# Performance work log

Hardware: AMD Instinct MI355X
Metric: run time of the kernel (lower is better)

## Reference

```python
import jax, jax.numpy as jnp
import numpy as np

N, E, B = 25600, 307200, 256
H, D, F0, K = 256, 16, 7, 6
GNN_OUT, TDA_IN, TDA_OUT, MEG_IN, MEG_OUT = 192, 32, 128, 16, 64
FUSION = GNN_OUT + TDA_OUT + MEG_OUT  # 384
MID = FUSION // 2  # 192


def _ln(x, g, b, eps=1e-5):
    m = x.mean(-1, keepdims=True)
    v = x.var(-1, keepdims=True)
    return (x - m) * jax.lax.rsqrt(v + eps) * g + b


def _ntn(x, pos, neg):
    return jnp.nan_to_num(x, nan=0.0, posinf=pos, neginf=neg)


def setup_inputs():
    key = jax.random.key(0)
    ks = iter(jax.random.split(key, 80))
    p = lambda *s: 0.05 * jax.random.normal(next(ks), s, jnp.float32)
    inp = {
        "x": jax.random.normal(next(ks), (N, F0), jnp.float32),
        "edge_attr": jax.random.uniform(next(ks), (E, D), dtype=jnp.float32),
        "tda": jax.random.normal(next(ks), (B, TDA_IN), jnp.float32),
        "megnet": jax.random.normal(next(ks), (B, MEG_IN), jnp.float32),
        "edge_index": jax.random.randint(next(ks), (2, E), 0, N),
        "batch": jnp.repeat(jnp.arange(B), N // B),
        # GNN encoder
        "gin_W": p(F0, H), "gin_b": jnp.zeros(H),
        "conv_Wf": p(6, 2 * H + D, H), "conv_bf": jnp.zeros((6, H)),
        "conv_Ws": p(6, 2 * H + D, H), "conv_bs": jnp.zeros((6, H)),
        "gln_g": jnp.ones((6, H)), "gln_b": jnp.zeros((6, H)),
        "gout_W": p(H, GNN_OUT), "gout_b": jnp.zeros(GNN_OUT),
        # TDA projector 32->256->256->128
        "t1_W": p(TDA_IN, 2 * TDA_OUT), "t1_b": jnp.zeros(2 * TDA_OUT),
        "tln1_g": jnp.ones(2 * TDA_OUT), "tln1_b": jnp.zeros(2 * TDA_OUT),
        "t2_W": p(2 * TDA_OUT, 2 * TDA_OUT), "t2_b": jnp.zeros(2 * TDA_OUT),
        "tln2_g": jnp.ones(2 * TDA_OUT), "tln2_b": jnp.zeros(2 * TDA_OUT),
        "t3_W": p(2 * TDA_OUT, TDA_OUT), "t3_b": jnp.zeros(TDA_OUT),
        # MEGNet projector 16->128->128->64
        "m1_W": p(MEG_IN, 2 * MEG_OUT), "m1_b": jnp.zeros(2 * MEG_OUT),
        "mln1_g": jnp.ones(2 * MEG_OUT), "mln1_b": jnp.zeros(2 * MEG_OUT),
        "m2_W": p(2 * MEG_OUT, 2 * MEG_OUT), "m2_b": jnp.zeros(2 * MEG_OUT),
        "mln2_g": jnp.ones(2 * MEG_OUT), "mln2_b": jnp.zeros(2 * MEG_OUT),
        "m3_W": p(2 * MEG_OUT, MEG_OUT), "m3_b": jnp.zeros(MEG_OUT),
        # fusion LN
        "fln_g": jnp.ones(FUSION), "fln_b": jnp.zeros(FUSION),
        # CPPN gate 384->48->24->6
        "g1_W": p(FUSION, K * 8), "g1_b": jnp.zeros(K * 8),
        "hln_g": jnp.ones(K * 8), "hln_b": jnp.zeros(K * 8),
        "g2_W": p(K * 8, K * 4), "g2_b": jnp.zeros(K * 4),
        "g3_W": p(K * 4, K), "g3_b": jnp.zeros(K),
        # CPPN poly branches stacked over K
        "plin_W": p(K, FUSION), "plin_b": jnp.zeros(K),
        "pq1_W": p(K, FUSION, MID), "pq1_b": jnp.zeros((K, MID)),
        "pq2_W": p(K, MID), "pq2_b": jnp.zeros(K),
        "pc1_W": p(K, FUSION, MID // 2), "pc1_b": jnp.zeros((K, MID // 2)),
        "pc2_W": p(K, MID // 2), "pc2_b": jnp.zeros(K),
    }
    return inp


def _forward(x, edge_attr, tda, megnet, edge_index, batch,
             gin_W, gin_b, conv_Wf, conv_bf, conv_Ws, conv_bs, gln_g, gln_b, gout_W, gout_b,
             t1_W, t1_b, tln1_g, tln1_b, t2_W, t2_b, tln2_g, tln2_b, t3_W, t3_b,
             m1_W, m1_b, mln1_g, mln1_b, m2_W, m2_b, mln2_g, mln2_b, m3_W, m3_b,
             fln_g, fln_b,
             g1_W, g1_b, hln_g, hln_b, g2_W, g2_b, g3_W, g3_b,
             plin_W, plin_b, pq1_W, pq1_b, pq2_W, pq2_b, pc1_W, pc1_b, pc2_W, pc2_b):
    silu = jax.nn.silu
    tda = _ntn(tda, 3.0, -3.0)
    megnet = _ntn(megnet, 3.0, -3.0)
    x = _ntn(x, 3.0, -3.0)
    ea = _ntn(edge_attr, 1.0, 0.0)
    src, dst = edge_index[0], edge_index[1]

    h = silu(x @ gin_W + gin_b)  # [N, H]
    for i in range(6):
        # CGConv message: z_ij = [x_i, x_j, e_ij]; sigmoid(z Wf) * softplus(z Ws); sum-agg + root
        z = jnp.concatenate([h[dst], h[src], ea], axis=-1)  # [E, 2H+D]
        msg = jax.nn.sigmoid(z @ conv_Wf[i] + conv_bf[i]) * jax.nn.softplus(z @ conv_Ws[i] + conv_bs[i])
        conv = h + jax.ops.segment_sum(msg, dst, num_segments=N)
        h = _ln(silu(conv) + h, gln_g[i], gln_b[i])
    cnt = jax.ops.segment_sum(jnp.ones((N, 1), h.dtype), batch, num_segments=B)
    pooled = jax.ops.segment_sum(h, batch, num_segments=B) / jnp.maximum(cnt, 1.0)
    z_gnn = jnp.nan_to_num(pooled @ gout_W + gout_b)  # [B, 192]

    # --- projectors ---
    a = _ln(silu(tda @ t1_W + t1_b), tln1_g, tln1_b)
    a = _ln(silu(a @ t2_W + t2_b), tln2_g, tln2_b)
    z_tda = jnp.nan_to_num(a @ t3_W + t3_b)  # [B, 128]
    m = _ln(silu(megnet @ m1_W + m1_b), mln1_g, mln1_b)
    m = _ln(silu(m @ m2_W + m2_b), mln2_g, mln2_b)
    z_meg = jnp.nan_to_num(m @ m3_W + m3_b)  # [B, 64]

    z = _ln(jnp.concatenate([z_gnn, z_tda, z_meg], axis=-1), fln_g, fln_b)  # [B, 384]

    # --- CPPN mixture head ---
    g = _ln(silu(z @ g1_W + g1_b), hln_g, hln_b)
    g = silu(g @ g2_W + g2_b)
    gates = jax.nn.softmax(g @ g3_W + g3_b, axis=-1)  # [B, K]
    lin = jnp.einsum('bd,kd->bk', z, plin_W) + plin_b
    hq = silu(jnp.einsum('bd,kdm->bkm', z, pq1_W) + pq1_b)  # [B, K, 192]
    q = jnp.einsum('bkm,km->bk', hq, pq2_W) + pq2_b
    hc = silu(jnp.einsum('bd,kdm->bkm', z, pc1_W) + pc1_b) ** 2  # [B, K, 96]
    c = jnp.einsum('bkm,km->bk', hc, pc2_W) + pc2_b
    y = (gates * (lin + q + c)).sum(-1)  # [B]
    return y, z


def reference(x, edge_attr, tda, megnet, edge_index, batch,
              gin_W, gin_b, conv_Wf, conv_bf, conv_Ws, conv_bs, gln_g, gln_b, gout_W, gout_b,
              t1_W, t1_b, tln1_g, tln1_b, t2_W, t2_b, tln2_g, tln2_b, t3_W, t3_b,
              m1_W, m1_b, mln1_g, mln1_b, m2_W, m2_b, mln2_g, mln2_b, m3_W, m3_b,
              fln_g, fln_b,
              g1_W, g1_b, hln_g, hln_b, g2_W, g2_b, g3_W, g3_b,
              plin_W, plin_b, pq1_W, pq1_b, pq2_W, pq2_b, pc1_W, pc1_b, pc2_W, pc2_b):
    return _forward(x, edge_attr, tda, megnet, edge_index, batch,
                    gin_W, gin_b, conv_Wf, conv_bf, conv_Ws, conv_bs, gln_g, gln_b, gout_W, gout_b,
                    t1_W, t1_b, tln1_g, tln1_b, t2_W, t2_b, tln2_g, tln2_b, t3_W, t3_b,
                    m1_W, m1_b, mln1_g, mln1_b, m2_W, m2_b, mln2_g, mln2_b, m3_W, m3_b,
                    fln_g, fln_b,
                    g1_W, g1_b, hln_g, hln_b, g2_W, g2_b, g3_W, g3_b,
                    plin_W, plin_b, pq1_W, pq1_b, pq2_W, pq2_b, pc1_W, pc1_b, pc2_W, pc2_b)
```

## Files before the change

### kernel.cpp

```cpp
#include <hip/hip_runtime.h>
#include <hip/hip_bf16.h>
#include <cmath>

#define NN 25600
#define NE 307200
#define NB 256
#define HD 256

typedef __attribute__((ext_vector_type(8))) short short8;
typedef __attribute__((ext_vector_type(4))) float f32x4;
typedef __attribute__((ext_vector_type(2))) float f32x2;
typedef __attribute__((ext_vector_type(2))) _Float16 h16x2;
typedef __attribute__((ext_vector_type(2))) __fp16 fp16x2;

__device__ __forceinline__ float ntn_f(float v, float pos, float neg) {
  if (isnan(v)) return 0.f;
  if (isinf(v)) return v > 0.f ? pos : neg;
  return v;
}
__device__ __forceinline__ float ntn_def(float v) {
  if (isnan(v)) return 0.f;
  if (isinf(v)) return v > 0.f ? 3.4028234663852886e38f : -3.4028234663852886e38f;
  return v;
}
__device__ __forceinline__ float sigmoid_f(float x) { return 1.f / (1.f + __expf(-x)); }
__device__ __forceinline__ float silu_f(float x) { return x * sigmoid_f(x); }
__device__ __forceinline__ float softplus_f(float x) {
  return fmaxf(x, 0.f) + __logf(1.f + __expf(-fabsf(x)));
}
__device__ __forceinline__ unsigned short f2bf(float f) {
  unsigned int u = __float_as_uint(f);
  u += 0x7fffu + ((u >> 16) & 1u);
  return (unsigned short)(u >> 16);
}
__device__ __forceinline__ float bflo(unsigned int u) { return __uint_as_float(u << 16); }
__device__ __forceinline__ float bfhi(unsigned int u) { return __uint_as_float(u & 0xffff0000u); }
__device__ __forceinline__ h16x2 u2h(unsigned int u) {
  union { unsigned int u; h16x2 h; } x; x.u = u; return x.h;
}
__device__ __forceinline__ unsigned int pk2u(float a, float b) {
  union { fp16x2 p; unsigned int u; } x;
  x.p = __builtin_amdgcn_cvt_pkrtz(a, b);
  return x.u;
}
#if __has_builtin(__builtin_amdgcn_fdot2)
#define FDOT2(a, b, c) __builtin_amdgcn_fdot2((a), (b), (c), false)
#else
__device__ __forceinline__ float fdot2_sw(h16x2 a, h16x2 b, float c) {
  return (float)a.x * (float)b.x + (float)a.y * (float)b.y + c;
}
#define FDOT2(a, b, c) fdot2_sw((a), (b), (c))
#endif

template <int NW>
__device__ __forceinline__ float blockSum(float v, float* sred) {
  int lane = threadIdx.x & 63, w = threadIdx.x >> 6;
#pragma unroll
  for (int o = 32; o; o >>= 1) v += __shfl_xor(v, o);
  __syncthreads();
  if (lane == 0) sred[w] = v;
  __syncthreads();
  float r = 0.f;
#pragma unroll
  for (int i = 0; i < NW; ++i) r += sred[i];
  return r;
}

__global__ void k_hist(const int* __restrict__ dst, int* __restrict__ counts, int E) {
  int e = blockIdx.x * 256 + threadIdx.x;
  if (e < E) atomicAdd(&counts[dst[e]], 1);
}

__global__ __launch_bounds__(1024) void k_scan(const int* __restrict__ counts,
                                               int* __restrict__ offs, int n) {
  __shared__ int sd[1024];
  __shared__ int run;
  int tid = threadIdx.x;
  if (tid == 0) run = 0;
  __syncthreads();
  for (int base = 0; base < n; base += 1024) {
    int i = base + tid;
    int v = (i < n) ? counts[i] : 0;
    sd[tid] = v;
    __syncthreads();
    int acc = v;
    for (int off = 1; off < 1024; off <<= 1) {
      int t = (tid >= off) ? sd[tid - off] : 0;
      __syncthreads();
      acc += t;
      sd[tid] = acc;
      __syncthreads();
    }
    int r = run;
    if (i < n) offs[i] = r + acc - v;
    __syncthreads();
    if (tid == 1023) run = r + sd[1023];
    __syncthreads();
  }
  if (threadIdx.x == 0) offs[n] = run;
}

__global__ void k_scatter(const int* __restrict__ dst, const int* __restrict__ offs,
                          int* __restrict__ cursor, int* __restrict__ eidx, int E) {
  int e = blockIdx.x * 256 + threadIdx.x;
  if (e < E) {
    int d = dst[e];
    int p = offs[d] + atomicAdd(&cursor[d], 1);
    eidx[p] = e;
  }
}

__global__ void k_srcperm(const int* __restrict__ eidx, const int* __restrict__ srcArr,
                          int* __restrict__ srcs, int E) {
  int i = blockIdx.x * 256 + threadIdx.x;
  if (i < E) srcs[i] = srcArr[eidx[i]];
}

__global__ void k_eapermh(const int* __restrict__ eidx, const float* __restrict__ ea,
                          unsigned int* __restrict__ eah, int E) {
  int gid = blockIdx.x * 256 + threadIdx.x;
  if (gid < E * 8) {
    int ii = gid >> 3, kp = gid & 7;
    int e = eidx[ii];
    float v0 = ea[(size_t)e * 16 + 2 * kp];
    float v1 = ea[(size_t)e * 16 + 2 * kp + 1];
    eah[gid] = pk2u(v0, v1);
  }
}

__global__ void k_pack(const float* __restrict__ conv_Wf, const float* __restrict__ conv_Ws,
                       unsigned short* __restrict__ w4t) {
  int layer = blockIdx.y;
  int gid = blockIdx.x * 256 + threadIdx.x;
  int k = gid & 255;
  int c = gid >> 8;
  int j = c & 255;
  int tbl = c >> 8;
  const float* W = (tbl < 2) ? conv_Wf : conv_Ws;
  int krow = (tbl & 1) ? 256 + k : k;
  float v = W[((size_t)layer * 528 + krow) * 256 + j];
  w4t[((size_t)layer * 1024 + c) * 256 + k] = f2bf(v);
}

__global__ void k_packEh(const float* __restrict__ conv_Wf, const float* __restrict__ conv_Ws,
                         unsigned int* __restrict__ wh) {
  int layer = blockIdx.y;
  int gid = blockIdx.x * 256 + threadIdx.x;
  int dp = gid >> 5, dw = gid & 31;
  int g = dw >> 4, dloc = (dw >> 3) & 1, kp = dw & 7;
  int d = dp * 2 + dloc;
  const float* W = g ? conv_Ws : conv_Wf;
  float v0 = W[((size_t)layer * 528 + 512 + 2 * kp) * 256 + d];
  float v1 = W[((size_t)layer * 528 + 512 + 2 * kp + 1) * 256 + d];
  wh[((size_t)layer * 128 + dp) * 32 + dw] = pk2u(v0, v1);
}

__global__ void k_gin(const float* __restrict__ x, const float* __restrict__ W,
                      const float* __restrict__ bias, float* __restrict__ h,
                      unsigned short* __restrict__ hbf) {
  int n = blockIdx.x, j = threadIdx.x;
  float xv[7];
#pragma unroll
  for (int k = 0; k < 7; ++k) xv[k] = ntn_f(x[n * 7 + k], 3.f, -3.f);
  float acc = bias[j];
#pragma unroll
  for (int k = 0; k < 7; ++k) acc += xv[k] * W[k * 256 + j];
  float o = silu_f(acc);
  h[(size_t)n * 256 + j] = o;
  hbf[(size_t)n * 256 + j] = f2bf(o);
}

__global__ __launch_bounds__(256) void k_gemm_bf16(
    const unsigned short* __restrict__ Abf,
    const unsigned short* __restrict__ w4t,
    const float* __restrict__ bf, const float* __restrict__ bs,
    unsigned short* __restrict__ Pout) {
  __shared__ unsigned short As[128 * 56];
  __shared__ unsigned short Bs[128 * 56];
  int tid = threadIdx.x;
  int lane = tid & 63, w = tid >> 6;
  int wr = w >> 1, wc = w & 1;
  int m0 = blockIdx.x * 128, n0 = blockIdx.y * 128;
  int l15 = lane & 15, l4 = lane >> 4;
  f32x4 acc[4][4];
#pragma unroll
  for (int i = 0; i < 4; ++i)
#pragma unroll
    for (int j = 0; j < 4; ++j) acc[i][j] = (f32x4)0.f;
  for (int kt = 0; kt < 8; ++kt) {
    int k0 = kt * 32;
    if (kt) __syncthreads();
#pragma unroll
    for (int c = 0; c < 2; ++c) {
      int chunk = tid + c * 256;
      int row = chunk >> 2, q = chunk & 3;
      *(uint4*)&As[row * 56 + q * 8] =
          *(const uint4*)&Abf[(size_t)(m0 + row) * 256 + k0 + q * 8];
      *(uint4*)&Bs[row * 56 + q * 8] =
          *(const uint4*)&w4t[(size_t)(n0 + row) * 256 + k0 + q * 8];
    }
    __syncthreads();
    short8 a[4], b[4];
#pragma unroll
    for (int f = 0; f < 4; ++f) {
      a[f] = *(const short8*)&As[(wr * 64 + f * 16 + l15) * 56 + l4 * 8];
      b[f] = *(const short8*)&Bs[(wc * 64 + f * 16 + l15) * 56 + l4 * 8];
    }
#pragma unroll
    for (int i = 0; i < 4; ++i)
#pragma unroll
      for (int j = 0; j < 4; ++j)
        acc[i][j] = __builtin_amdgcn_mfma_f32_16x16x32_bf16(a[i], b[j], acc[i][j], 0, 0, 0);
  }
#pragma unroll
  for (int j = 0; j < 4; ++j) {
    int gcol = n0 + wc * 64 + j * 16 + l15;
    float bias = (gcol < 256) ? bf[gcol] : (gcol >= 512 && gcol < 768) ? bs[gcol - 512] : 0.f;
#pragma unroll
    for (int i = 0; i < 4; ++i) {
#pragma unroll
      for (int r = 0; r < 4; ++r) {
        int grow = m0 + wr * 64 + i * 16 + l4 * 4 + r;
        Pout[(size_t)grow * 1024 + gcol] = f2bf(acc[i][j][r] + bias);
      }
    }
  }
}

__global__ __launch_bounds__(256) void k_edge3(
    const float* __restrict__ h, const unsigned short* __restrict__ P,
    const unsigned int* __restrict__ eah,
    const int* __restrict__ srcs, const int* __restrict__ offs,
    const unsigned int* __restrict__ wh,
    const float* __restrict__ lng, const float* __restrict__ lnb,
    float* __restrict__ hout, unsigned short* __restrict__ hbfout) {
  __shared__ float sr1[4], sr2[4];
  int tid = threadIdx.x, lane = tid & 63, w = tid >> 6;
  int n = blockIdx.x * 2 + (w >> 1);
  int half = w & 1;
  int idx = half * 128 + lane * 2;
  int dp = half * 64 + lane;

  unsigned int wk[32];
  {
    const uint4* wb = (const uint4*)(wh + (size_t)dp * 32);
#pragma unroll
    for (int q = 0; q < 8; ++q) {
      uint4 t = wb[q];
      wk[q * 4 + 0] = t.x; wk[q * 4 + 1] = t.y;
      wk[q * 4 + 2] = t.z; wk[q * 4 + 3] = t.w;
    }
  }
#pragma unroll
  for (int q = 0; q < 32; ++q) asm volatile("" : "+v"(wk[q]));

  f32x2 lg = *(const f32x2*)(lng + idx);
  f32x2 lb = *(const f32x2*)(lnb + idx);
  const unsigned short* Pn = P + (size_t)n * 1024;
  unsigned int ud0 = *(const unsigned int*)(Pn + idx);
  unsigned int ud1 = *(const unsigned int*)(Pn + 512 + idx);
  float pf0 = bflo(ud0), pf1 = bfhi(ud0);
  float ps0 = bflo(ud1), ps1 = bfhi(ud1);
  f32x2 hn = *(const f32x2*)(h + (size_t)n * 256 + idx);
  float acc0 = 0.f, acc1 = 0.f;
  int e0 = __builtin_amdgcn_readfirstlane(offs[n]);
  int e1 = __builtin_amdgcn_readfirstlane(offs[n + 1]);

  for (int ii = e0; ii < e1; ++ii) {
    int s = srcs[ii];
    const unsigned short* Ps = P + (size_t)s * 1024;
    unsigned int uf = *(const unsigned int*)(Ps + 256 + idx);
    unsigned int us = *(const unsigned int*)(Ps + 768 + idx);
    const uint4* e4 = (const uint4*)(eah + (size_t)ii * 8);
    uint4 ea0 = e4[0], ea1 = e4[1];
    unsigned int ec[8] = {ea0.x, ea0.y, ea0.z, ea0.w, ea1.x, ea1.y, ea1.z, ea1.w};
    float af0 = pf0, af1 = pf1, as0 = ps0, as1 = ps1;
#pragma unroll
    for (int kp = 0; kp < 8; ++kp) {
      h16x2 c = u2h(ec[kp]);
      af0 = FDOT2(u2h(wk[kp]), c, af0);
      af1 = FDOT2(u2h(wk[8 + kp]), c, af1);
      as0 = FDOT2(u2h(wk[16 + kp]), c, as0);
      as1 = FDOT2(u2h(wk[24 + kp]), c, as1);
    }
    af0 += bflo(uf); af1 += bfhi(uf);
    as0 += bflo(us); as1 += bfhi(us);
    acc0 += sigmoid_f(af0) * softplus_f(as0);
    acc1 += sigmoid_f(af1) * softplus_f(as1);
  }
  float cv0 = hn.x + acc0;
  float cv1 = hn.y + acc1;
  float t0 = silu_f(cv0) + hn.x;
  float t1 = silu_f(cv1) + hn.y;
  float s1 = t0 + t1, s2 = t0 * t0 + t1 * t1;
#pragma unroll
  for (int o = 32; o; o >>= 1) {
    s1 += __shfl_xor(s1, o);
    s2 += __shfl_xor(s2, o);
  }
  if (lane == 0) { sr1[w] = s1; sr2[w] = s2; }
  __syncthreads();
  int pw = w ^ 1;
  float S1 = sr1[w] + sr1[pw];
  float S2 = sr2[w] + sr2[pw];
  float mean = S1 * (1.f / 256.f);
  float var = S2 * (1.f / 256.f) - mean * mean;
  float inv = rsqrtf(var + 1e-5f);
  float o0 = (t0 - mean) * inv * lg.x + lb.x;
  float o1 = (t1 - mean) * inv * lg.y + lb.y;
  f32x2 ov; ov.x = o0; ov.y = o1;
  *(f32x2*)(hout + (size_t)n * 256 + idx) = ov;
  unsigned int pk = (unsigned int)f2bf(o0) | ((unsigned int)f2bf(o1) << 16);
  *(unsigned int*)(hbfout + (size_t)n * 256 + idx) = pk;
}

__global__ __launch_bounds__(256) void k_pool2(const float* __restrict__ h,
                                               float* __restrict__ pooled) {
  int b = blockIdx.x, j = threadIdx.x;
  const float* hp = h + (size_t)b * 100 * 256 + j;
  float s = 0.f;
  for (int i = 0; i < 100; ++i) s += hp[(size_t)i * 256];
  pooled[b * 256 + j] = s * 0.01f;
}

__global__ void k_zgnn(const float* __restrict__ pooled,
                       const float* __restrict__ W, const float* __restrict__ bias,
                       float* __restrict__ zf) {
  int b = blockIdx.x, j = threadIdx.x;
  float acc = bias[j];
  for (int k = 0; k < 256; ++k) acc += pooled[b * 256 + k] * W[k * 192 + j];
  zf[b * 384 + j] = ntn_def(acc);
}

__global__ __launch_bounds__(256) void k_tda(const float* __restrict__ tda,
    const float* __restrict__ W1, const float* __restrict__ b1,
    const float* __restrict__ g1, const float* __restrict__ bb1,
    const float* __restrict__ W2, const float* __restrict__ b2,
    const float* __restrict__ g2, const float* __restrict__ bb2,
    const float* __restrict__ W3, const float* __restrict__ b3, float* __restrict__ zf) {
  __shared__ float sin_[32];
  __shared__ float sa[256];
  __shared__ float sred[4];
  int b = blockIdx.x, tid = threadIdx.x;
  if (tid < 32) sin_[tid] = ntn_f(tda[b * 32 + tid], 3.f, -3.f);
  __syncthreads();
  float v = b1[tid];
#pragma unroll
  for (int k = 0; k < 32; ++k) v += sin_[k] * W1[k * 256 + tid];
  v = silu_f(v);
  float s1 = blockSum<4>(v, sred);
  float s2 = blockSum<4>(v * v, sred);
  float mean = s1 * (1.f / 256.f), var = s2 * (1.f / 256.f) - mean * mean;
  float inv = rsqrtf(var + 1e-5f);
  v = (v - mean) * inv * g1[tid] + bb1[tid];
  sa[tid] = v;
  __syncthreads();
  float v2 = b2[tid];
  for (int k = 0; k < 256; ++k) v2 += sa[k] * W2[k * 256 + tid];
  v2 = silu_f(v2);
  s1 = blockSum<4>(v2, sred);
  s2 = blockSum<4>(v2 * v2, sred);
  mean = s1 * (1.f / 256.f); var = s2 * (1.f / 256.f) - mean * mean;
  inv = rsqrtf(var + 1e-5f);
  v2 = (v2 - mean) * inv * g2[tid] + bb2[tid];
  __syncthreads();
  sa[tid] = v2;
  __syncthreads();
  if (tid < 128) {
    float o = b3[tid];
    for (int k = 0; k < 256; ++k) o += sa[k] * W3[k * 128 + tid];
    zf[b * 384 + 192 + tid] = ntn_def(o);
  }
}

__global__ __launch_bounds__(128) void k_meg(const float* __restrict__ mg,
    const float* __restrict__ W1, const float* __restrict__ b1,
    const float* __restrict__ g1, const float* __restrict__ bb1,
    const float* __restrict__ W2, const float* __restrict__ b2,
    const float* __restrict__ g2, const float* __restrict__ bb2,
    const float* __restrict__ W3, const float* __restrict__ b3, float* __restrict__ zf) {
  __shared__ float sin_[16];
  __shared__ float sa[128];
  __shared__ float sred[2];
  int b = blockIdx.x, tid = threadIdx.x;
  if (tid < 16) sin_[tid] = ntn_f(mg[b * 16 + tid], 3.f, -3.f);
  __syncthreads();
  float v = b1[tid];
#pragma unroll
  for (int k = 0; k < 16; ++k) v += sin_[k] * W1[k * 128 + tid];
  v = silu_f(v);
  float s1 = blockSum<2>(v, sred);
  float s2 = blockSum<2>(v * v, sred);
  float mean = s1 * (1.f / 128.f), var = s2 * (1.f / 128.f) - mean * mean;
  float inv = rsqrtf(var + 1e-5f);
  v = (v - mean) * inv * g1[tid] + bb1[tid];
  sa[tid] = v;
  __syncthreads();
  float v2 = b2[tid];
  for (int k = 0; k < 128; ++k) v2 += sa[k] * W2[k * 128 + tid];
  v2 = silu_f(v2);
  s1 = blockSum<2>(v2, sred);
  s2 = blockSum<2>(v2 * v2, sred);
  mean = s1 * (1.f / 128.f); var = s2 * (1.f / 128.f) - mean * mean;
  inv = rsqrtf(var + 1e-5f);
  v2 = (v2 - mean) * inv * g2[tid] + bb2[tid];
  __syncthreads();
  sa[tid] = v2;
  __syncthreads();
  if (tid < 64) {
    float o = b3[tid];
    for (int k = 0; k < 128; ++k) o += sa[k] * W3[k * 64 + tid];
    zf[b * 384 + 320 + tid] = ntn_def(o);
  }
}

__global__ __launch_bounds__(384) void k_cppn(const float* __restrict__ zf,
    const float* __restrict__ flng, const float* __restrict__ flnb,
    const float* __restrict__ g1W, const float* __restrict__ g1b,
    const float* __restrict__ hg, const float* __restrict__ hb,
    const float* __restrict__ g2W, const float* __restrict__ g2b,
    const float* __restrict__ g3W, const float* __restrict__ g3b,
    const float* __restrict__ plW, const float* __restrict__ plb,
    const float* __restrict__ pq1W, const float* __restrict__ pq1b,
    const float* __restrict__ pq2W, const float* __restrict__ pq2b,
    const float* __restrict__ pc1W, const float* __restrict__ pc1b,
    const float* __restrict__ pc2W, const float* __restrict__ pc2b,
    float* __restrict__ zout, float* __restrict__ y) {
  __shared__ float sz[384];
  __shared__ float sred[6];
  __shared__ float sg[48];
  __shared__ float s24[24];
  __shared__ float gates[6];
  __shared__ float lin[6];
  __shared__ float qv[6], cvv[6];
  __shared__ float mn48, iv48;
  __shared__ float prodq[1152];
  __shared__ float prodc[576];
  int b = blockIdx.x, tid = threadIdx.x;
  int lane = tid & 63, wv = tid >> 6;

  float v = zf[(size_t)b * 384 + tid];
  float s1 = blockSum<6>(v, sred);
  float s2 = blockSum<6>(v * v, sred);
  float mean = s1 * (1.f / 384.f), var = s2 * (1.f / 384.f) - mean * mean;
  float inv = rsqrtf(var + 1e-5f);
  float zv = (v - mean) * inv * flng[tid] + flnb[tid];
  sz[tid] = zv;
  zout[(size_t)b * 384 + tid] = zv;
  __syncthreads();

  {
    int j = tid >> 3, p = tid & 7;
    float a = 0.f;
    for (int d = p; d < 384; d += 8) a += sz[d] * g1W[d * 48 + j];
    a += __shfl_xor(a, 1);
    a += __shfl_xor(a, 2);
    a += __shfl_xor(a, 4);
    if (p == 0) sg[j] = silu_f(a + g1b[j]);
  }
  __syncthreads();
  if (tid < 64) {
    float x = (tid < 48) ? sg[tid] : 0.f;
    float t1 = x, t2 = x * x;
#pragma unroll
    for (int o = 32; o; o >>= 1) {
      t1 += __shfl_xor(t1, o);
      t2 += __shfl_xor(t2, o);
    }
    if (tid == 0) {
      mn48 = t1 * (1.f / 48.f);
      float vr = t2 * (1.f / 48.f) - mn48 * mn48;
      iv48 = rsqrtf(vr + 1e-5f);
    }
  }
  __syncthreads();
  if (tid < 48) sg[tid] = (sg[tid] - mn48) * iv48 * hg[tid] + hb[tid];
  __syncthreads();
  {
    int j = tid >> 4, p = tid & 15;
    int d0 = p * 3;
    float a = sg[d0] * g2W[d0 * 24 + j] + sg[d0 + 1] * g2W[(d0 + 1) * 24 + j] +
              sg[d0 + 2] * g2W[(d0 + 2) * 24 + j];
    a += __shfl_xor(a, 1);
    a += __shfl_xor(a, 2);
    a += __shfl_xor(a, 4);
    a += __shfl_xor(a, 8);
    if (p == 0) s24[j] = silu_f(a + g2b[j]);
  }
  __syncthreads();
  if (tid < 6) {
    float a = g3b[tid];
    for (int k = 0; k < 24; ++k) a += s24[k] * g3W[k * 6 + tid];
    gates[tid] = a;
  }
  __syncthreads();
  if (tid == 0) {
    float mx = gates[0];
    for (int i = 1; i < 6; ++i) mx = fmaxf(mx, gates[i]);
    float s = 0.f;
    for (int i = 0; i < 6; ++i) { gates[i] = __expf(gates[i] - mx); s += gates[i]; }
    float rs = 1.f / s;
    for (int i = 0; i < 6; ++i) gates[i] *= rs;
  }
  {
    float p = 0.f;
    for (int d = lane; d < 384; d += 64) p += sz[d] * plW[wv * 384 + d];
#pragma unroll
    for (int o = 32; o; o >>= 1) p += __shfl_xor(p, o);
    if (lane == 0) lin[wv] = p + plb[wv];
  }
  if (tid < 288) {
    int k = tid / 48, m4 = (tid % 48) * 4;
    f32x4 a = (f32x4)0.f;
    const float* Wp = pq1W + (size_t)k * 384 * 192 + m4;
    for (int d = 0; d < 384; ++d) {
      float4 w4 = *(const float4*)(Wp + (size_t)d * 192);
      float zd = sz[d];
      a.x += zd * w4.x; a.y += zd * w4.y; a.z += zd * w4.z; a.w += zd * w4.w;
    }
#pragma unroll
    for (int r = 0; r < 4; ++r) {
      int m = m4 + r;
      prodq[k * 192 + m] = silu_f(a[r] + pq1b[k * 192 + m]) * pq2W[k * 192 + m];
    }
  }
  if (tid < 144) {
    int k = tid / 24, m4 = (tid % 24) * 4;
    f32x4 a = (f32x4)0.f;
    const float* Wp = pc1W + (size_t)k * 384 * 96 + m4;
    for (int d = 0; d < 384; ++d) {
      float4 w4 = *(const float4*)(Wp + (size_t)d * 96);
      float zd = sz[d];
      a.x += zd * w4.x; a.y += zd * w4.y; a.z += zd * w4.z; a.w += zd * w4.w;
    }
#pragma unroll
    for (int r = 0; r < 4; ++r) {
      int m = m4 + r;
      float sl = silu_f(a[r] + pc1b[k * 96 + m]);
      prodc[k * 96 + m] = sl * sl * pc2W[k * 96 + m];
    }
  }
  __syncthreads();
  {
    float s = prodq[wv * 192 + lane] + prodq[wv * 192 + 64 + lane] +
              prodq[wv * 192 + 128 + lane];
#pragma unroll
    for (int o = 32; o; o >>= 1) s += __shfl_xor(s, o);
    if (lane == 0) qv[wv] = s + pq2b[wv];
    float c = prodc[wv * 96 + lane];
    float c2 = (lane < 32) ? prodc[wv * 96 + 64 + lane] : 0.f;
    float sc = c + c2;
#pragma unroll
    for (int o = 32; o; o >>= 1) sc += __shfl_xor(sc, o);
    if (lane == 0) cvv[wv] = sc + pc2b[wv];
  }
  __syncthreads();
  if (tid == 0) {
    float yy = 0.f;
    for (int k = 0; k < 6; ++k) yy += gates[k] * (lin[k] + qv[k] + cvv[k]);
    y[b] = yy;
  }
}

extern "C" void kernel_launch(void* const* d_in, const int* in_sizes, int n_in,
                              void* d_out, int out_size, void* d_ws, size_t ws_size,
                              hipStream_t stream) {
  const float* x         = (const float*)d_in[0];
  const float* edge_attr = (const float*)d_in[1];
  const float* tda       = (const float*)d_in[2];
  const float* megnet    = (const float*)d_in[3];
  const int*   edge_index= (const int*)d_in[4];
  const float* gin_W = (const float*)d_in[6];
  const float* gin_b = (const float*)d_in[7];
  const float* conv_Wf = (const float*)d_in[8];
  const float* conv_bf = (const float*)d_in[9];
  const float* conv_Ws = (const float*)d_in[10];
  const float* conv_bs = (const float*)d_in[11];
  const float* gln_g = (const float*)d_in[12];
  const float* gln_b = (const float*)d_in[13];
  const float* gout_W = (const float*)d_in[14];
  const float* gout_b = (const float*)d_in[15];
  const float* t1_W = (const float*)d_in[16];
  const float* t1_b = (const float*)d_in[17];
  const float* tln1_g = (const float*)d_in[18];
  const float* tln1_b = (const float*)d_in[19];
  const float* t2_W = (const float*)d_in[20];
  const float* t2_b = (const float*)d_in[21];
  const float* tln2_g = (const float*)d_in[22];
  const float* tln2_b = (const float*)d_in[23];
  const float* t3_W = (const float*)d_in[24];
  const float* t3_b = (const float*)d_in[25];
  const float* m1_W = (const float*)d_in[26];
  const float* m1_b = (const float*)d_in[27];
  const float* mln1_g = (const float*)d_in[28];
  const float* mln1_b = (const float*)d_in[29];
  const float* m2_W = (const float*)d_in[30];
  const float* m2_b = (const float*)d_in[31];
  const float* mln2_g = (const float*)d_in[32];
  const float* mln2_b = (const float*)d_in[33];
  const float* m3_W = (const float*)d_in[34];
  const float* m3_b = (const float*)d_in[35];
  const float* fln_g = (const float*)d_in[36];
  const float* fln_b = (const float*)d_in[37];
  const float* g1_W = (const float*)d_in[38];
  const float* g1_b = (const float*)d_in[39];
  const float* hln_g = (const float*)d_in[40];
  const float* hln_b = (const float*)d_in[41];
  const float* g2_W = (const float*)d_in[42];
  const float* g2_b = (const float*)d_in[43];
  const float* g3_W = (const float*)d_in[44];
  const float* g3_b = (const float*)d_in[45];
  const float* plin_W = (const float*)d_in[46];
  const float* plin_b = (const float*)d_in[47];
  const float* pq1_W = (const float*)d_in[48];
  const float* pq1_b = (const float*)d_in[49];
  const float* pq2_W = (const float*)d_in[50];
  const float* pq2_b = (const float*)d_in[51];
  const float* pc1_W = (const float*)d_in[52];
  const float* pc1_b = (const float*)d_in[53];
  const float* pc2_W = (const float*)d_in[54];
  const float* pc2_b = (const float*)d_in[55];

  float* ws = (float*)d_ws;
  float* hA = ws;
  float* hB = hA + (size_t)NN * 256;
  float* pooled = hB + (size_t)NN * 256;
  float* zf = pooled + (size_t)NB * 256;
  unsigned short* hbfA = (unsigned short*)(zf + (size_t)NB * 384);
  unsigned short* hbfB = hbfA + (size_t)NN * 256;
  unsigned short* Pbf = hbfB + (size_t)NN * 256;
  unsigned short* w4t = Pbf + (size_t)NN * 1024;
  unsigned int* wh6 = (unsigned int*)(w4t + (size_t)6 * 1024 * 256);
  unsigned int* eah = wh6 + (size_t)6 * 128 * 32;
  int* counts = (int*)(eah + (size_t)NE * 8);
  int* cursor = counts + NN;
  int* offs = cursor + NN;
  int* eidx = offs + NN + 1;
  int* srcs = eidx + NE;

  const int* srcArr = edge_index;
  const int* dstArr = edge_index + NE;

  hipMemsetAsync(counts, 0, (size_t)2 * NN * sizeof(int), stream);

  k_hist<<<(NE + 255) / 256, 256, 0, stream>>>(dstArr, counts, NE);
  k_scan<<<1, 1024, 0, stream>>>(counts, offs, NN);
  k_scatter<<<(NE + 255) / 256, 256, 0, stream>>>(dstArr, offs, cursor, eidx, NE);
  k_srcperm<<<(NE + 255) / 256, 256, 0, stream>>>(eidx, srcArr, srcs, NE);
  k_eapermh<<<(NE * 8 + 255) / 256, 256, 0, stream>>>(eidx, edge_attr, eah, NE);
  k_pack<<<dim3(1024, 6), 256, 0, stream>>>(conv_Wf, conv_Ws, w4t);
  k_packEh<<<dim3(16, 6), 256, 0, stream>>>(conv_Wf, conv_Ws, wh6);

  k_gin<<<NN, 256, 0, stream>>>(x, gin_W, gin_b, hA, hbfA);

  float* hcur = hA;          float* hnext = hB;
  unsigned short* bcur = hbfA; unsigned short* bnext = hbfB;
  for (int i = 0; i < 6; ++i) {
    k_gemm_bf16<<<dim3(NN / 128, 8), 256, 0, stream>>>(
        bcur, w4t + (size_t)i * 1024 * 256, conv_bf + i * 256, conv_bs + i * 256, Pbf);
    k_edge3<<<NN / 2, 256, 0, stream>>>(hcur, Pbf, eah, srcs, offs,
                                        wh6 + (size_t)i * 128 * 32,
                                        gln_g + i * 256, gln_b + i * 256, hnext, bnext);
    float* tf = hcur; hcur = hnext; hnext = tf;
    unsigned short* tb = bcur; bcur = bnext; bnext = tb;
  }

  k_pool2<<<NB, 256, 0, stream>>>(hcur, pooled);
  k_zgnn<<<NB, 192, 0, stream>>>(pooled, gout_W, gout_b, zf);
  k_tda<<<NB, 256, 0, stream>>>(tda, t1_W, t1_b, tln1_g, tln1_b, t2_W, t2_b, tln2_g, tln2_b,
                                t3_W, t3_b, zf);
  k_meg<<<NB, 128, 0, stream>>>(megnet, m1_W, m1_b, mln1_g, mln1_b, m2_W, m2_b, mln2_g, mln2_b,
                                m3_W, m3_b, zf);

  float* yout = (float*)d_out;
  float* zout = yout + NB;
  k_cppn<<<NB, 384, 0, stream>>>(zf, fln_g, fln_b,
                                 g1_W, g1_b, hln_g, hln_b, g2_W, g2_b, g3_W, g3_b,
                                 plin_W, plin_b, pq1_W, pq1_b, pq2_W, pq2_b,
                                 pc1_W, pc1_b, pc2_W, pc2_b, zout, yout);
}
```

Before: 1.323 ms.

## Map one node per block with one channel per thread in edge kernel

Restructures the edge aggregation kernel so each 256-thread block handles a single node and each thread owns one channel, instead of two nodes per block with two channels per thread. The edge-attribute weight table is repacked per channel (16 words instead of 32), which halves the per-thread register footprint and drops the asm register pinning. The cost is twice as many blocks, narrower 16-bit gathers of the P rows, and a redundant edge-attribute load per extra wave for each edge.

```diff
diff --git a/kernel.cpp b/kernel.cpp
--- a/kernel.cpp
+++ b/kernel.cpp
@@ -33,8 +33,9 @@
   u += 0x7fffu + ((u >> 16) & 1u);
   return (unsigned short)(u >> 16);
 }
-__device__ __forceinline__ float bflo(unsigned int u) { return __uint_as_float(u << 16); }
-__device__ __forceinline__ float bfhi(unsigned int u) { return __uint_as_float(u & 0xffff0000u); }
+__device__ __forceinline__ float bfu(unsigned short u) {
+  return __uint_as_float((unsigned int)u << 16);
+}
 __device__ __forceinline__ h16x2 u2h(unsigned int u) {
   union { unsigned int u; h16x2 h; } x; x.u = u; return x.h;
 }
@@ -142,17 +143,16 @@
   w4t[((size_t)layer * 1024 + c) * 256 + k] = f2bf(v);
 }
 
-__global__ void k_packEh(const float* __restrict__ conv_Wf, const float* __restrict__ conv_Ws,
-                         unsigned int* __restrict__ wh) {
+__global__ void k_packEd(const float* __restrict__ conv_Wf, const float* __restrict__ conv_Ws,
+                         unsigned int* __restrict__ whd) {
   int layer = blockIdx.y;
   int gid = blockIdx.x * 256 + threadIdx.x;
-  int dp = gid >> 5, dw = gid & 31;
-  int g = dw >> 4, dloc = (dw >> 3) & 1, kp = dw & 7;
-  int d = dp * 2 + dloc;
+  int d = gid >> 4, pr = gid & 15;
+  int g = pr >> 3, kp = pr & 7;
   const float* W = g ? conv_Ws : conv_Wf;
   float v0 = W[((size_t)layer * 528 + 512 + 2 * kp) * 256 + d];
   float v1 = W[((size_t)layer * 528 + 512 + 2 * kp + 1) * 256 + d];
-  wh[((size_t)layer * 128 + dp) * 32 + dw] = pk2u(v0, v1);
+  whd[((size_t)layer * 256 + d) * 16 + pr] = pk2u(v0, v1);
 }
 
 __global__ void k_gin(const float* __restrict__ x, const float* __restrict__ W,
@@ -227,72 +227,59 @@
   }
 }
 
-__global__ __launch_bounds__(256) void k_edge3(
+__global__ __launch_bounds__(256) void k_edge4(
     const float* __restrict__ h, const unsigned short* __restrict__ P,
     const unsigned int* __restrict__ eah,
     const int* __restrict__ srcs, const int* __restrict__ offs,
-    const unsigned int* __restrict__ wh,
+    const unsigned int* __restrict__ whd,
     const float* __restrict__ lng, const float* __restrict__ lnb,
     float* __restrict__ hout, unsigned short* __restrict__ hbfout) {
   __shared__ float sr1[4], sr2[4];
   int tid = threadIdx.x, lane = tid & 63, w = tid >> 6;
-  int n = blockIdx.x * 2 + (w >> 1);
-  int half = w & 1;
-  int idx = half * 128 + lane * 2;
-  int dp = half * 64 + lane;
-
-  unsigned int wk[32];
+  int n = blockIdx.x;
+  int d = w * 64 + lane;
+
+  unsigned int wk[16];
   {
-    const uint4* wb = (const uint4*)(wh + (size_t)dp * 32);
-#pragma unroll
-    for (int q = 0; q < 8; ++q) {
+    const uint4* wb = (const uint4*)(whd + (size_t)d * 16);
+#pragma unroll
+    for (int q = 0; q < 4; ++q) {
       uint4 t = wb[q];
       wk[q * 4 + 0] = t.x; wk[q * 4 + 1] = t.y;
       wk[q * 4 + 2] = t.z; wk[q * 4 + 3] = t.w;
     }
   }
-#pragma unroll
-  for (int q = 0; q < 32; ++q) asm volatile("" : "+v"(wk[q]));
-
-  f32x2 lg = *(const f32x2*)(lng + idx);
-  f32x2 lb = *(const f32x2*)(lnb + idx);
+  float lg = lng[d], lb = lnb[d];
   const unsigned short* Pn = P + (size_t)n * 1024;
-  unsigned int ud0 = *(const unsigned int*)(Pn + idx);
-  unsigned int ud1 = *(const unsigned int*)(Pn + 512 + idx);
-  float pf0 = bflo(ud0), pf1 = bfhi(ud0);
-  float ps0 = bflo(ud1), ps1 = bfhi(ud1);
-  f32x2 hn = *(const f32x2*)(h + (size_t)n * 256 + idx);
-  float acc0 = 0.f, acc1 = 0.f;
+  float pfd = bfu(Pn[d]);
+  float psd = bfu(Pn[512 + d]);
+  float hn = h[(size_t)n * 256 + d];
+  float acc = 0.f;
   int e0 = __builtin_amdgcn_readfirstlane(offs[n]);
   int e1 = __builtin_amdgcn_readfirstlane(offs[n + 1]);
 
   for (int ii = e0; ii < e1; ++ii) {
     int s = srcs[ii];
     const unsigned short* Ps = P + (size_t)s * 1024;
-    unsigned int uf = *(const unsigned int*)(Ps + 256 + idx);
-    unsigned int us = *(const unsigned int*)(Ps + 768 + idx);
+    unsigned short uf = Ps[256 + d];
+    unsigned short us = Ps[768 + d];
     const uint4* e4 = (const uint4*)(eah + (size_t)ii * 8);
     uint4 ea0 = e4[0], ea1 = e4[1];
     unsigned int ec[8] = {ea0.x, ea0.y, ea0.z, ea0.w, ea1.x, ea1.y, ea1.z, ea1.w};
-    float af0 = pf0, af1 = pf1, as0 = ps0, as1 = ps1;
+    float af = pfd, as_ = psd;
 #pragma unroll
     for (int kp = 0; kp < 8; ++kp) {
       h16x2 c = u2h(ec[kp]);
-      af0 = FDOT2(u2h(wk[kp]), c, af0);
-      af1 = FDOT2(u2h(wk[8 + kp]), c, af1);
-      as0 = FDOT2(u2h(wk[16 + kp]), c, as0);
-      as1 = FDOT2(u2h(wk[24 + kp]), c, as1);
-    }
-    af0 += bflo(uf); af1 += bfhi(uf);
-    as0 += bflo(us); as1 += bfhi(us);
-    acc0 += sigmoid_f(af0) * softplus_f(as0);
-    acc1 += sigmoid_f(af1) * softplus_f(as1);
-  }
-  float cv0 = hn.x + acc0;
-  float cv1 = hn.y + acc1;
-  float t0 = silu_f(cv0) + hn.x;
-  float t1 = silu_f(cv1) + hn.y;
-  float s1 = t0 + t1, s2 = t0 * t0 + t1 * t1;
+      af = FDOT2(u2h(wk[kp]), c, af);
+      as_ = FDOT2(u2h(wk[8 + kp]), c, as_);
+    }
+    af += bfu(uf);
+    as_ += bfu(us);
+    acc += sigmoid_f(af) * softplus_f(as_);
+  }
+  float cv = hn + acc;
+  float t = silu_f(cv) + hn;
+  float s1 = t, s2 = t * t;
 #pragma unroll
   for (int o = 32; o; o >>= 1) {
     s1 += __shfl_xor(s1, o);
@@ -300,18 +287,14 @@
   }
   if (lane == 0) { sr1[w] = s1; sr2[w] = s2; }
   __syncthreads();
-  int pw = w ^ 1;
-  float S1 = sr1[w] + sr1[pw];
-  float S2 = sr2[w] + sr2[pw];
+  float S1 = sr1[0] + sr1[1] + sr1[2] + sr1[3];
+  float S2 = sr2[0] + sr2[1] + sr2[2] + sr2[3];
   float mean = S1 * (1.f / 256.f);
   float var = S2 * (1.f / 256.f) - mean * mean;
   float inv = rsqrtf(var + 1e-5f);
-  float o0 = (t0 - mean) * inv * lg.x + lb.x;
-  float o1 = (t1 - mean) * inv * lg.y + lb.y;
-  f32x2 ov; ov.x = o0; ov.y = o1;
-  *(f32x2*)(hout + (size_t)n * 256 + idx) = ov;
-  unsigned int pk = (unsigned int)f2bf(o0) | ((unsigned int)f2bf(o1) << 16);
-  *(unsigned int*)(hbfout + (size_t)n * 256 + idx) = pk;
+  float o0 = (t - mean) * inv * lg + lb;
+  hout[(size_t)n * 256 + d] = o0;
+  hbfout[(size_t)n * 256 + d] = f2bf(o0);
 }
 
 __global__ __launch_bounds__(256) void k_pool2(const float* __restrict__ h,
@@ -630,8 +613,8 @@
   unsigned short* hbfB = hbfA + (size_t)NN * 256;
   unsigned short* Pbf = hbfB + (size_t)NN * 256;
   unsigned short* w4t = Pbf + (size_t)NN * 1024;
-  unsigned int* wh6 = (unsigned int*)(w4t + (size_t)6 * 1024 * 256);
-  unsigned int* eah = wh6 + (size_t)6 * 128 * 32;
+  unsigned int* whd6 = (unsigned int*)(w4t + (size_t)6 * 1024 * 256);
+  unsigned int* eah = whd6 + (size_t)6 * 256 * 16;
   int* counts = (int*)(eah + (size_t)NE * 8);
   int* cursor = counts + NN;
   int* offs = cursor + NN;
@@ -649,7 +632,7 @@
   k_srcperm<<<(NE + 255) / 256, 256, 0, stream>>>(eidx, srcArr, srcs, NE);
   k_eapermh<<<(NE * 8 + 255) / 256, 256, 0, stream>>>(eidx, edge_attr, eah, NE);
   k_pack<<<dim3(1024, 6), 256, 0, stream>>>(conv_Wf, conv_Ws, w4t);
-  k_packEh<<<dim3(16, 6), 256, 0, stream>>>(conv_Wf, conv_Ws, wh6);
+  k_packEd<<<dim3(16, 6), 256, 0, stream>>>(conv_Wf, conv_Ws, whd6);
 
   k_gin<<<NN, 256, 0, stream>>>(x, gin_W, gin_b, hA, hbfA);
 
@@ -658,9 +641,9 @@
   for (int i = 0; i < 6; ++i) {
     k_gemm_bf16<<<dim3(NN / 128, 8), 256, 0, stream>>>(
         bcur, w4t + (size_t)i * 1024 * 256, conv_bf + i * 256, conv_bs + i * 256, Pbf);
-    k_edge3<<<NN / 2, 256, 0, stream>>>(hcur, Pbf, eah, srcs, offs,
-                                        wh6 + (size_t)i * 128 * 32,
-                                        gln_g + i * 256, gln_b + i * 256, hnext, bnext);
+    k_edge4<<<NN, 256, 0, stream>>>(hcur, Pbf, eah, srcs, offs,
+                                    whd6 + (size_t)i * 256 * 16,
+                                    gln_g + i * 256, gln_b + i * 256, hnext, bnext);
     float* tf = hcur; hcur = hnext; hnext = tf;
     unsigned short* tb = bcur; bcur = bnext; bnext = tb;
   }
```

Measured after the change: 1.199 ms. 1.1x faster.
